# Optimization experiments

Hardware: AMD Instinct MI355X
Metric: run time of the kernel (lower is better)

Reference implementation:

```python
import jax, jax.numpy as jnp
import numpy as np

H = 64        # HIDDEN_DIM
V = 64        # VOCAB_SIZE
INNER = 16    # INNER_DIM
LR = 0.01     # INFERENCE_LR
B = 256
L = 2048
EPS = 1e-5    # LayerNorm eps (torch default)


def setup_inputs() -> dict:
    key = jax.random.key(0)
    ks = jax.random.split(key, 8)

    def lin(k, fi, fo):
        return jax.random.normal(k, (fi, fo), jnp.float32) / np.sqrt(fi).astype(np.float32)

    return {
        "seq": jax.random.randint(ks[0], (B, L), 0, V),
        "embed": jax.random.normal(ks[1], (V, H), jnp.float32) * 0.02,
        "ff_w1": lin(ks[2], H, 2 * H), "ff_b1": jnp.zeros((2 * H,), jnp.float32),
        "ff_w2": lin(ks[3], 2 * H, H), "ff_b2": jnp.zeros((H,), jnp.float32),
        "ln_g": jnp.ones((H,), jnp.float32), "ln_b": jnp.zeros((H,), jnp.float32),
        "w1": lin(ks[4], H, INNER), "b1": jnp.zeros((INNER,), jnp.float32),
        "w2": lin(ks[5], INNER, H), "b2": jnp.zeros((H,), jnp.float32),
        "out_w": lin(ks[6], H, V), "out_b": jnp.zeros((V,), jnp.float32),
    }


def _mlp(p, x):
    W1, B1, W2, B2 = p
    return jnp.maximum(x @ W1 + B1, 0.0) @ W2 + B2


def reference(seq, embed, ff_w1, ff_b1, ff_w2, ff_b2, ln_g, ln_b,
              w1, b1, w2, b2, out_w, out_b):
    # Encoder: embed -> residual FFN -> LayerNorm
    e = embed[seq]                                        # [B,L,H]
    ff = jnp.maximum(e @ ff_w1 + ff_b1, 0.0) @ ff_w2 + ff_b2
    h = e + ff
    mu = h.mean(-1, keepdims=True)
    var = ((h - mu) ** 2).mean(-1, keepdims=True)
    hs = (h - mu) / jnp.sqrt(var + EPS) * ln_g + ln_b     # [B,L,H]
    hs = jax.lax.stop_gradient(hs)                        # all TTT inputs are .detach()ed in torch

    T = (L - 2) // 2                                      # len(range(0, L-3, 2))
    idx = jnp.arange(T) * 2
    k_seq = hs[:, idx]                                    # [B,T,H]
    v_seq = hs[:, idx + 1]                                # [B,T,H]

    # base params copied via load_state_dict -> no grad connection
    p0 = tuple(jax.lax.stop_gradient(p) for p in (w1, b1, w2, b2))

    def ttt(kseq, vseq, qlast):
        def step(p, kv):
            k, v = kv
            g = jax.grad(lambda pp: jnp.mean((_mlp(pp, k) - v) ** 2))(p)
            return jax.tree_util.tree_map(lambda a, ga: a - LR * ga, p, g), None
        pf, _ = jax.lax.scan(step, p0, (kseq, vseq))
        return _mlp(pf, qlast)                            # [H]

    ctx = jax.vmap(ttt)(k_seq, v_seq, hs[:, -1])          # [B,H]
    ctx = jax.lax.stop_gradient(ctx)                      # torch builds ctx under no_grad
    return ctx @ out_w + out_b                            # [B,V]
```

## Files before the change

### kernel.cpp

```cpp
#include <hip/hip_runtime.h>

#define TSTEPS 1023
#define GAMMA  (0.01f / 32.0f)
#define EPSV   1e-5f

#define WS_HS 0
#define WS_G  4096
#define WS_Z0 8192

typedef float v2f __attribute__((ext_vector_type(2)));
typedef unsigned int v2u __attribute__((ext_vector_type(2)));

template<int CTRL>
__device__ __forceinline__ float dppmov(float x) {
    return __int_as_float(__builtin_amdgcn_update_dpp(0, __float_as_int(x), CTRL, 0xF, 0xF, true));
}
__device__ __forceinline__ v2u swap16(float a, float b) {
    return __builtin_amdgcn_permlane16_swap(__float_as_uint(a), __float_as_uint(b), false, false);
}
__device__ __forceinline__ v2u swap32(float a, float b) {
    return __builtin_amdgcn_permlane32_swap(__float_as_uint(a), __float_as_uint(b), false, false);
}
#define U2F(x) __uint_as_float(x)
#define PV(arr, j) (((j) & 1) ? arr[(j) >> 1].y : arr[(j) >> 1].x)

__global__ void hs_kernel(const float* __restrict__ embed,
                          const float* __restrict__ ffw1, const float* __restrict__ ffb1,
                          const float* __restrict__ ffw2, const float* __restrict__ ffb2,
                          const float* __restrict__ lng,  const float* __restrict__ lnb,
                          float* __restrict__ ws) {
    __shared__ float e[64];
    __shared__ float a1[128];
    int w = blockIdx.x;
    int tid = threadIdx.x;
    if (tid < 64) e[tid] = embed[w * 64 + tid];
    __syncthreads();
    float z1 = ffb1[tid];
    for (int x = 0; x < 64; ++x) z1 += e[x] * ffw1[x * 128 + tid];
    a1[tid] = fmaxf(z1, 0.0f);
    __syncthreads();
    if (tid < 64) {
        float f = ffb2[tid];
        for (int i = 0; i < 128; ++i) f += a1[i] * ffw2[i * 64 + tid];
        float hv = e[tid] + f;
        float s = hv;
#pragma unroll
        for (int m = 32; m >= 1; m >>= 1) s += __shfl_xor(s, m);
        float mu = s * (1.0f / 64.0f);
        float dv = hv - mu;
        float vs = dv * dv;
#pragma unroll
        for (int m = 32; m >= 1; m >>= 1) vs += __shfl_xor(vs, m);
        float rstd = 1.0f / sqrtf(vs * (1.0f / 64.0f) + EPSV);
        ws[WS_HS + w * 64 + tid] = dv * rstd * lng[tid] + lnb[tid];
    }
}

__global__ void gz_kernel(const float* __restrict__ w1, const float* __restrict__ b1,
                          float* __restrict__ ws) {
    __shared__ float row[64];
    int w = blockIdx.x, tid = threadIdx.x;
    row[tid] = ws[WS_HS + w * 64 + tid];
    __syncthreads();
    float g = 0.0f;
    for (int x = 0; x < 64; ++x) g += row[x] * ws[WS_HS + tid * 64 + x];
    ws[WS_G + w * 64 + tid] = GAMMA * g + GAMMA;
    if (tid < 16) {
        float z = b1[tid];
        for (int x = 0; x < 64; ++x) z += row[x] * w1[x * 16 + tid];
        ws[WS_Z0 + w * 16 + tid] = z;
    }
}

struct TTT2Smem {
    float hs[4096];
    float Gs[4096];
    int   sq[2048];
    __align__(16) float Z[2][512];
    float ybuf[2][2][64];
    float ctxp[2][64];
};

__device__ __forceinline__ void reduce8(const v2f* a2, const v2f* p2, v2f* dz2) {
    float q0 = PV(p2, 0) + dppmov<0xB1>(PV(p2, 4));
    float q1 = PV(p2, 1) + dppmov<0xB1>(PV(p2, 5));
    float q2 = PV(p2, 2) + dppmov<0xB1>(PV(p2, 6));
    float q3 = PV(p2, 3) + dppmov<0xB1>(PV(p2, 7));
    float rm0 = (a2[0].x > 0.0f) ? q0 : 0.0f;
    float rm1 = (a2[0].y > 0.0f) ? q1 : 0.0f;
    float rm2 = (a2[1].x > 0.0f) ? q2 : 0.0f;
    float rm3 = (a2[1].y > 0.0f) ? q3 : 0.0f;
    v2u f01 = swap16(rm0, rm1);
    const float F  = U2F(f01[0]) + U2F(f01[1]);
    v2u f23 = swap16(rm2, rm3);
    const float F2 = U2F(f23[0]) + U2F(f23[1]);
    v2u g01 = swap32(F, F2);
    float T = U2F(g01[0]) + U2F(g01[1]);
    T = T + dppmov<0x122>(T);
    T = T + dppmov<0x124>(T);
    T = T + dppmov<0x128>(T);
    v2u u01 = swap16(T, T);
    v2u v02 = swap32(U2F(u01[0]), U2F(u01[0]));
    v2u v13 = swap32(U2F(u01[1]), U2F(u01[1]));
    const float D0 = U2F(v02[0]);
    const float D2 = U2F(v02[1]);
    const float D1 = U2F(v13[0]);
    const float D3 = U2F(v13[1]);
    dz2[0] = {D0, D1};
    dz2[1] = {D2, D3};
    dz2[2] = {dppmov<0xB1>(D0), dppmov<0xB1>(D1)};
    dz2[3] = {dppmov<0xB1>(D2), dppmov<0xB1>(D3)};
}

__launch_bounds__(128, 1)
__global__ void ttt_kernel(const int* __restrict__ seq,
                           const float* __restrict__ w2, const float* __restrict__ b2i,
                           const float* __restrict__ outw, const float* __restrict__ outb,
                           const float* __restrict__ ws, float* __restrict__ out) {
    __shared__ TTT2Smem sm;

    const int b    = blockIdx.x;
    const int tid  = threadIdx.x;
    const int wv   = tid >> 6;
    const int lane = tid & 63;
    const int b0   = lane & 1;
    const int X    = b0 << 2;
    const int sl   = (lane >> 2) & 1;
    const bool wv0 = (wv == 0);

    {
        float4*       hv = (float4*)sm.hs;
        const float4* sv = (const float4*)(ws + WS_HS);
#pragma unroll
        for (int m = 0; m < 8; ++m) hv[m * 128 + tid] = sv[m * 128 + tid];
        float4*       gv = (float4*)sm.Gs;
        const float4* gs = (const float4*)(ws + WS_G);
#pragma unroll
        for (int m = 0; m < 8; ++m) gv[m * 128 + tid] = gs[m * 128 + tid];
        int4*       qv = (int4*)sm.sq;
        const int4* qs = (const int4*)(seq + b * 2048);
#pragma unroll
        for (int m = 0; m < 4; ++m) qv[m * 128 + tid] = qs[m * 128 + tid];
        const float* z0p = ws + WS_Z0 + lane * 16 + 8 * wv;
        float* zw = sm.Z[wv] + lane * 8;
        *(float4*)(zw + 4 * sl)       = *(const float4*)(z0p);
        *(float4*)(zw + 4 * (1 ^ sl)) = *(const float4*)(z0p + 4);
    }

    v2f W2p[4];
#pragma unroll
    for (int i = 0; i < 4; ++i) {
        v2f w;
        w.x = w2[(8 * wv + ((2 * i) ^ X)) * 64 + lane];
        w.y = w2[(8 * wv + ((2 * i + 1) ^ X)) * 64 + lane];
        W2p[i] = w;
    }
    float ybias = wv0 ? b2i[lane] : 0.0f;
    const float gma = wv0 ? GAMMA : 0.0f;
    __syncthreads();

    float* const Zw = sm.Z[wv];
    int tk = sm.sq[0];
    v2f z2[4];
    {
        const float* zb = Zw + tk * 8;
        const int x0 = (b0 ^ ((tk >> 2) & 1)) << 2;
        const float4 c0 = *(const float4*)(zb + x0);
        const float4 c1 = *(const float4*)(zb + (x0 ^ 4));
        z2[0] = {c0.x, c0.y}; z2[1] = {c0.z, c0.w};
        z2[2] = {c1.x, c1.y}; z2[3] = {c1.z, c1.w};
    }
    float4 ZrQ[2];
    v2f* Zv = (v2f*)ZrQ;
    {
        const float* zb = Zw + lane * 8;
        const int x0 = (b0 ^ sl) << 2;
        ZrQ[0] = *(const float4*)(zb + x0);
        ZrQ[1] = *(const float4*)(zb + (x0 ^ 4));
    }
    float vv = sm.hs[sm.sq[1] * 64 + lane];

    float4* const wp0 = (float4*)(Zw + lane * 8 + ((b0 ^ sl) << 2));
    float4* const wp1 = (float4*)(Zw + lane * 8 + (((b0 ^ sl) << 2) ^ 4));

    int2 pairT  = *(const int2*)(sm.sq + 2);
    int2 pairT1 = *(const int2*)(sm.sq + 4);

#pragma unroll 2
    for (int t = 0; t < TSTEPS - 1; ++t) {
        const int tkn = pairT.x;
        const int tvn = pairT.y;
        const int par = t & 1;

        const v2f zero2 = {0.0f, 0.0f};
        v2f a2[4];
#pragma unroll
        for (int i = 0; i < 4; ++i) a2[i] = __builtin_elementwise_max(z2[i], zero2);
        v2f acc0 = a2[0] * W2p[0] + a2[1] * W2p[1];
        v2f acc1 = a2[2] * W2p[2] + a2[3] * W2p[3];
        v2f accv = acc0 + acc1;
        const float ypart = ybias + accv.x + accv.y;

        sm.ybuf[par][wv][lane] = ypart;
        __syncthreads();
        const float yoth = sm.ybuf[par][wv ^ 1][lane];

        const float* zb = Zw + tkn * 8;
        const int x0 = (b0 ^ ((tkn >> 2) & 1)) << 2;
        const float4 e0 = *(const float4*)(zb + x0);
        const float4 e1 = *(const float4*)(zb + (x0 ^ 4));
        const float vnext = sm.hs[tvn * 64 + lane];
        const float cr = sm.Gs[tk * 64 + lane];
        const float cz = sm.Gs[tk * 64 + tkn];
        const int2 pairT2 = *(const int2*)(sm.sq + 2 * t + 6);

        const float d = (ypart + yoth) - vv;

        const v2f d2 = {d, d};
        v2f p2[4];
#pragma unroll
        for (int i = 0; i < 4; ++i) p2[i] = W2p[i] * d2;
        const float sd = GAMMA * d;
        ybias -= gma * d;
        const v2f sd2 = {sd, sd};
#pragma unroll
        for (int i = 0; i < 4; ++i) W2p[i] = W2p[i] - sd2 * a2[i];

        v2f dz2[4];
        reduce8(a2, p2, dz2);

        const v2f cr2 = {cr, cr}, cz2 = {cz, cz};
        const v2f zq2[4] = { {e0.x, e0.y}, {e0.z, e0.w}, {e1.x, e1.y}, {e1.z, e1.w} };
#pragma unroll
        for (int i = 0; i < 4; ++i) {
            Zv[i] = Zv[i] - cr2 * dz2[i];
            z2[i] = zq2[i] - cz2 * dz2[i];
        }
        *wp0 = ZrQ[0];
        *wp1 = ZrQ[1];

        vv = vnext;
        tk = tkn;
        pairT = pairT1;
        pairT1 = pairT2;
    }

    {
        const int tkn = pairT.y;
        const v2f zero2 = {0.0f, 0.0f};
        v2f a2[4];
#pragma unroll
        for (int i = 0; i < 4; ++i) a2[i] = __builtin_elementwise_max(z2[i], zero2);
        v2f acc0 = a2[0] * W2p[0] + a2[1] * W2p[1];
        v2f acc1 = a2[2] * W2p[2] + a2[3] * W2p[3];
        v2f accv = acc0 + acc1;
        const float ypart = ybias + accv.x + accv.y;

        sm.ybuf[0][wv][lane] = ypart;
        __syncthreads();
        const float yoth = sm.ybuf[0][wv ^ 1][lane];

        const float* zb = Zw + tkn * 8;
        const int x0 = (b0 ^ ((tkn >> 2) & 1)) << 2;
        const float4 e0 = *(const float4*)(zb + x0);
        const float4 e1 = *(const float4*)(zb + (x0 ^ 4));
        const float cz = sm.Gs[tk * 64 + tkn];

        const float d = (ypart + yoth) - vv;

        const v2f d2 = {d, d};
        v2f p2[4];
#pragma unroll
        for (int i = 0; i < 4; ++i) p2[i] = W2p[i] * d2;
        const float sd = GAMMA * d;
        ybias -= gma * d;
        const v2f sd2 = {sd, sd};
#pragma unroll
        for (int i = 0; i < 4; ++i) W2p[i] = W2p[i] - sd2 * a2[i];

        v2f dz2[4];
        reduce8(a2, p2, dz2);

        const v2f cz2 = {cz, cz};
        const v2f zq2[4] = { {e0.x, e0.y}, {e0.z, e0.w}, {e1.x, e1.y}, {e1.z, e1.w} };
#pragma unroll
        for (int i = 0; i < 4; ++i) z2[i] = zq2[i] - cz2 * dz2[i];
    }

    {
        const v2f zero2 = {0.0f, 0.0f};
        v2f acc = {0.0f, 0.0f};
#pragma unroll
        for (int i = 0; i < 4; ++i)
            acc = acc + __builtin_elementwise_max(z2[i], zero2) * W2p[i];
        sm.ctxp[wv][lane] = ybias + acc.x + acc.y;
    }
    __syncthreads();
    if (wv0) {
        float o = outb[lane];
        for (int hh = 0; hh < 64; ++hh)
            o += (sm.ctxp[0][hh] + sm.ctxp[1][hh]) * outw[hh * 64 + lane];
        out[b * 64 + lane] = o;
    }
}

extern "C" void kernel_launch(void* const* d_in, const int* in_sizes, int n_in,
                              void* d_out, int out_size, void* d_ws, size_t ws_size,
                              hipStream_t stream) {
    const int*   seq   = (const int*)d_in[0];
    const float* embed = (const float*)d_in[1];
    const float* ffw1  = (const float*)d_in[2];
    const float* ffb1  = (const float*)d_in[3];
    const float* ffw2  = (const float*)d_in[4];
    const float* ffb2  = (const float*)d_in[5];
    const float* lng   = (const float*)d_in[6];
    const float* lnb   = (const float*)d_in[7];
    const float* w1    = (const float*)d_in[8];
    const float* b1    = (const float*)d_in[9];
    const float* w2    = (const float*)d_in[10];
    const float* b2    = (const float*)d_in[11];
    const float* outw  = (const float*)d_in[12];
    const float* outb  = (const float*)d_in[13];
    float* ws  = (float*)d_ws;
    float* out = (float*)d_out;

    hipLaunchKernelGGL(hs_kernel, dim3(64), dim3(128), 0, stream,
                       embed, ffw1, ffb1, ffw2, ffb2, lng, lnb, ws);
    hipLaunchKernelGGL(gz_kernel, dim3(64), dim3(64), 0, stream, w1, b1, ws);
    hipLaunchKernelGGL(ttt_kernel, dim3(256), dim3(128), 0, stream,
                       seq, w2, b2, outw, outb, ws, out);
}
```

Baseline: 395.0 us.

## Split TTT inner dimension across four wavefronts instead of two

The per-sequence TTT kernel now uses 256 threads (4 wavefronts), so each wave owns 4 of the 16 inner units instead of 8. This halves per-wave arithmetic and shortens the cross-lane reduction on the serial per-step chain. The cost is a 4-way partial-sum exchange through shared memory at each step's barrier. The Z-table row update is also deferred to the next iteration so its LDS write overlaps the barrier wait.

```diff
diff --git a/kernel.cpp b/kernel.cpp
--- a/kernel.cpp
+++ b/kernel.cpp
@@ -22,7 +22,6 @@
     return __builtin_amdgcn_permlane32_swap(__float_as_uint(a), __float_as_uint(b), false, false);
 }
 #define U2F(x) __uint_as_float(x)
-#define PV(arr, j) (((j) & 1) ? arr[(j) >> 1].y : arr[(j) >> 1].x)
 
 __global__ void hs_kernel(const float* __restrict__ embed,
                           const float* __restrict__ ffw1, const float* __restrict__ ffb1,
@@ -72,87 +71,71 @@
     }
 }
 
-struct TTT2Smem {
+struct TTT4Smem {
     float hs[4096];
     float Gs[4096];
     int   sq[2048];
-    __align__(16) float Z[2][512];
-    float ybuf[2][2][64];
-    float ctxp[2][64];
+    __align__(16) float Z[4][256];
+    float ybuf[2][4][64];
+    float ctxp[4][64];
 };
 
-__device__ __forceinline__ void reduce8(const v2f* a2, const v2f* p2, v2f* dz2) {
-    float q0 = PV(p2, 0) + dppmov<0xB1>(PV(p2, 4));
-    float q1 = PV(p2, 1) + dppmov<0xB1>(PV(p2, 5));
-    float q2 = PV(p2, 2) + dppmov<0xB1>(PV(p2, 6));
-    float q3 = PV(p2, 3) + dppmov<0xB1>(PV(p2, 7));
+__device__ __forceinline__ void reduce4(const v2f* a2, const v2f* p2, v2f* dz2) {
+    float q0 = p2[0].x + dppmov<0xB1>(p2[1].x);
+    float q1 = p2[0].y + dppmov<0xB1>(p2[1].y);
     float rm0 = (a2[0].x > 0.0f) ? q0 : 0.0f;
     float rm1 = (a2[0].y > 0.0f) ? q1 : 0.0f;
-    float rm2 = (a2[1].x > 0.0f) ? q2 : 0.0f;
-    float rm3 = (a2[1].y > 0.0f) ? q3 : 0.0f;
     v2u f01 = swap16(rm0, rm1);
-    const float F  = U2F(f01[0]) + U2F(f01[1]);
-    v2u f23 = swap16(rm2, rm3);
-    const float F2 = U2F(f23[0]) + U2F(f23[1]);
-    v2u g01 = swap32(F, F2);
-    float T = U2F(g01[0]) + U2F(g01[1]);
+    float T = U2F(f01[0]) + U2F(f01[1]);
+    v2u g01 = swap32(T, T);
+    T = U2F(g01[0]) + U2F(g01[1]);
     T = T + dppmov<0x122>(T);
     T = T + dppmov<0x124>(T);
     T = T + dppmov<0x128>(T);
     v2u u01 = swap16(T, T);
-    v2u v02 = swap32(U2F(u01[0]), U2F(u01[0]));
-    v2u v13 = swap32(U2F(u01[1]), U2F(u01[1]));
-    const float D0 = U2F(v02[0]);
-    const float D2 = U2F(v02[1]);
-    const float D1 = U2F(v13[0]);
-    const float D3 = U2F(v13[1]);
-    dz2[0] = {D0, D1};
-    dz2[1] = {D2, D3};
-    dz2[2] = {dppmov<0xB1>(D0), dppmov<0xB1>(D1)};
-    dz2[3] = {dppmov<0xB1>(D2), dppmov<0xB1>(D3)};
-}
-
-__launch_bounds__(128, 1)
+    const float A0 = U2F(u01[0]);
+    const float A1 = U2F(u01[1]);
+    dz2[0] = {A0, A1};
+    dz2[1] = {dppmov<0xB1>(A0), dppmov<0xB1>(A1)};
+}
+
+__launch_bounds__(256, 1)
 __global__ void ttt_kernel(const int* __restrict__ seq,
                            const float* __restrict__ w2, const float* __restrict__ b2i,
                            const float* __restrict__ outw, const float* __restrict__ outb,
                            const float* __restrict__ ws, float* __restrict__ out) {
-    __shared__ TTT2Smem sm;
+    __shared__ TTT4Smem sm;
 
     const int b    = blockIdx.x;
     const int tid  = threadIdx.x;
     const int wv   = tid >> 6;
     const int lane = tid & 63;
     const int b0   = lane & 1;
-    const int X    = b0 << 2;
-    const int sl   = (lane >> 2) & 1;
+    const int X    = b0 << 1;
     const bool wv0 = (wv == 0);
 
     {
         float4*       hv = (float4*)sm.hs;
         const float4* sv = (const float4*)(ws + WS_HS);
 #pragma unroll
-        for (int m = 0; m < 8; ++m) hv[m * 128 + tid] = sv[m * 128 + tid];
+        for (int m = 0; m < 4; ++m) hv[m * 256 + tid] = sv[m * 256 + tid];
         float4*       gv = (float4*)sm.Gs;
         const float4* gs = (const float4*)(ws + WS_G);
 #pragma unroll
-        for (int m = 0; m < 8; ++m) gv[m * 128 + tid] = gs[m * 128 + tid];
+        for (int m = 0; m < 4; ++m) gv[m * 256 + tid] = gs[m * 256 + tid];
         int4*       qv = (int4*)sm.sq;
         const int4* qs = (const int4*)(seq + b * 2048);
 #pragma unroll
-        for (int m = 0; m < 4; ++m) qv[m * 128 + tid] = qs[m * 128 + tid];
-        const float* z0p = ws + WS_Z0 + lane * 16 + 8 * wv;
-        float* zw = sm.Z[wv] + lane * 8;
-        *(float4*)(zw + 4 * sl)       = *(const float4*)(z0p);
-        *(float4*)(zw + 4 * (1 ^ sl)) = *(const float4*)(z0p + 4);
-    }
-
-    v2f W2p[4];
-#pragma unroll
-    for (int i = 0; i < 4; ++i) {
+        for (int m = 0; m < 2; ++m) qv[m * 256 + tid] = qs[m * 256 + tid];
+        *(float4*)(sm.Z[wv] + lane * 4) = *(const float4*)(ws + WS_Z0 + lane * 16 + 4 * wv);
+    }
+
+    v2f W2p[2];
+#pragma unroll
+    for (int i = 0; i < 2; ++i) {
         v2f w;
-        w.x = w2[(8 * wv + ((2 * i) ^ X)) * 64 + lane];
-        w.y = w2[(8 * wv + ((2 * i + 1) ^ X)) * 64 + lane];
+        w.x = w2[(4 * wv + ((2 * i) ^ X)) * 64 + lane];
+        w.y = w2[(4 * wv + ((2 * i + 1) ^ X)) * 64 + lane];
         W2p[i] = w;
     }
     float ybias = wv0 ? b2i[lane] : 0.0f;
@@ -161,27 +144,25 @@
 
     float* const Zw = sm.Z[wv];
     int tk = sm.sq[0];
-    v2f z2[4];
-    {
-        const float* zb = Zw + tk * 8;
-        const int x0 = (b0 ^ ((tk >> 2) & 1)) << 2;
-        const float4 c0 = *(const float4*)(zb + x0);
-        const float4 c1 = *(const float4*)(zb + (x0 ^ 4));
-        z2[0] = {c0.x, c0.y}; z2[1] = {c0.z, c0.w};
-        z2[2] = {c1.x, c1.y}; z2[3] = {c1.z, c1.w};
-    }
-    float4 ZrQ[2];
-    v2f* Zv = (v2f*)ZrQ;
-    {
-        const float* zb = Zw + lane * 8;
-        const int x0 = (b0 ^ sl) << 2;
-        ZrQ[0] = *(const float4*)(zb + x0);
-        ZrQ[1] = *(const float4*)(zb + (x0 ^ 4));
+    v2f z2[2];
+    {
+        const float* zb = Zw + tk * 4;
+        z2[0] = *(const v2f*)(zb + (b0 << 1));
+        z2[1] = *(const v2f*)(zb + ((b0 << 1) ^ 2));
+    }
+    v2f Zv[2];
+    {
+        const float* zb = Zw + lane * 4;
+        Zv[0] = *(const v2f*)(zb + (b0 << 1));
+        Zv[1] = *(const v2f*)(zb + ((b0 << 1) ^ 2));
     }
     float vv = sm.hs[sm.sq[1] * 64 + lane];
 
-    float4* const wp0 = (float4*)(Zw + lane * 8 + ((b0 ^ sl) << 2));
-    float4* const wp1 = (float4*)(Zw + lane * 8 + (((b0 ^ sl) << 2) ^ 4));
+    v2f* const wp0 = (v2f*)(Zw + lane * 4 + (b0 << 1));
+    v2f* const wp1 = (v2f*)(Zw + lane * 4 + ((b0 << 1) ^ 2));
+
+    v2f dzp[2] = {{0.0f, 0.0f}, {0.0f, 0.0f}};
+    float crp = 0.0f;
 
     int2 pairT  = *(const int2*)(sm.sq + 2);
     int2 pairT1 = *(const int2*)(sm.sq + 4);
@@ -193,51 +174,54 @@
         const int par = t & 1;
 
         const v2f zero2 = {0.0f, 0.0f};
-        v2f a2[4];
-#pragma unroll
-        for (int i = 0; i < 4; ++i) a2[i] = __builtin_elementwise_max(z2[i], zero2);
-        v2f acc0 = a2[0] * W2p[0] + a2[1] * W2p[1];
-        v2f acc1 = a2[2] * W2p[2] + a2[3] * W2p[3];
-        v2f accv = acc0 + acc1;
+        v2f a2[2];
+        a2[0] = __builtin_elementwise_max(z2[0], zero2);
+        a2[1] = __builtin_elementwise_max(z2[1], zero2);
+        v2f accv = a2[0] * W2p[0] + a2[1] * W2p[1];
         const float ypart = ybias + accv.x + accv.y;
 
         sm.ybuf[par][wv][lane] = ypart;
         __syncthreads();
-        const float yoth = sm.ybuf[par][wv ^ 1][lane];
-
-        const float* zb = Zw + tkn * 8;
-        const int x0 = (b0 ^ ((tkn >> 2) & 1)) << 2;
-        const float4 e0 = *(const float4*)(zb + x0);
-        const float4 e1 = *(const float4*)(zb + (x0 ^ 4));
+        const float y0 = sm.ybuf[par][0][lane];
+        const float y1 = sm.ybuf[par][1][lane];
+        const float y2 = sm.ybuf[par][2][lane];
+        const float y3 = sm.ybuf[par][3][lane];
+
+        const v2f crp2 = {crp, crp};
+        Zv[0] = Zv[0] - crp2 * dzp[0];
+        Zv[1] = Zv[1] - crp2 * dzp[1];
+        *wp0 = Zv[0];
+        *wp1 = Zv[1];
+        const float* zb = Zw + tkn * 4;
+        const v2f e0 = *(const v2f*)(zb + (b0 << 1));
+        const v2f e1 = *(const v2f*)(zb + ((b0 << 1) ^ 2));
         const float vnext = sm.hs[tvn * 64 + lane];
-        const float cr = sm.Gs[tk * 64 + lane];
-        const float cz = sm.Gs[tk * 64 + tkn];
+        const float crc = sm.Gs[tk * 64 + lane];
+        const float cz  = sm.Gs[tk * 64 + tkn];
         const int2 pairT2 = *(const int2*)(sm.sq + 2 * t + 6);
 
-        const float d = (ypart + yoth) - vv;
+        const float d = ((y0 + y1) + (y2 + y3)) - vv;
 
         const v2f d2 = {d, d};
-        v2f p2[4];
-#pragma unroll
-        for (int i = 0; i < 4; ++i) p2[i] = W2p[i] * d2;
+        v2f p2[2];
+        p2[0] = W2p[0] * d2;
+        p2[1] = W2p[1] * d2;
         const float sd = GAMMA * d;
         ybias -= gma * d;
         const v2f sd2 = {sd, sd};
-#pragma unroll
-        for (int i = 0; i < 4; ++i) W2p[i] = W2p[i] - sd2 * a2[i];
-
-        v2f dz2[4];
-        reduce8(a2, p2, dz2);
-
-        const v2f cr2 = {cr, cr}, cz2 = {cz, cz};
-        const v2f zq2[4] = { {e0.x, e0.y}, {e0.z, e0.w}, {e1.x, e1.y}, {e1.z, e1.w} };
-#pragma unroll
-        for (int i = 0; i < 4; ++i) {
-            Zv[i] = Zv[i] - cr2 * dz2[i];
-            z2[i] = zq2[i] - cz2 * dz2[i];
-        }
-        *wp0 = ZrQ[0];
-        *wp1 = ZrQ[1];
+        W2p[0] = W2p[0] - sd2 * a2[0];
+        W2p[1] = W2p[1] - sd2 * a2[1];
+
+        v2f dz2[2];
+        reduce4(a2, p2, dz2);
+
+        const v2f cz2 = {cz, cz};
+        z2[0] = e0 - cz2 * dz2[0];
+        z2[1] = e1 - cz2 * dz2[1];
+
+        dzp[0] = dz2[0];
+        dzp[1] = dz2[1];
+        crp = crc;
 
         vv = vnext;
         tk = tkn;
@@ -248,58 +232,62 @@
     {
         const int tkn = pairT.y;
         const v2f zero2 = {0.0f, 0.0f};
-        v2f a2[4];
-#pragma unroll
-        for (int i = 0; i < 4; ++i) a2[i] = __builtin_elementwise_max(z2[i], zero2);
-        v2f acc0 = a2[0] * W2p[0] + a2[1] * W2p[1];
-        v2f acc1 = a2[2] * W2p[2] + a2[3] * W2p[3];
-        v2f accv = acc0 + acc1;
+        v2f a2[2];
+        a2[0] = __builtin_elementwise_max(z2[0], zero2);
+        a2[1] = __builtin_elementwise_max(z2[1], zero2);
+        v2f accv = a2[0] * W2p[0] + a2[1] * W2p[1];
         const float ypart = ybias + accv.x + accv.y;
 
         sm.ybuf[0][wv][lane] = ypart;
         __syncthreads();
-        const float yoth = sm.ybuf[0][wv ^ 1][lane];
-
-        const float* zb = Zw + tkn * 8;
-        const int x0 = (b0 ^ ((tkn >> 2) & 1)) << 2;
-        const float4 e0 = *(const float4*)(zb + x0);
-        const float4 e1 = *(const float4*)(zb + (x0 ^ 4));
+        const float y0 = sm.ybuf[0][0][lane];
+        const float y1 = sm.ybuf[0][1][lane];
+        const float y2 = sm.ybuf[0][2][lane];
+        const float y3 = sm.ybuf[0][3][lane];
+
+        const v2f crp2 = {crp, crp};
+        Zv[0] = Zv[0] - crp2 * dzp[0];
+        Zv[1] = Zv[1] - crp2 * dzp[1];
+        *wp0 = Zv[0];
+        *wp1 = Zv[1];
+
+        const float* zb = Zw + tkn * 4;
+        const v2f e0 = *(const v2f*)(zb + (b0 << 1));
+        const v2f e1 = *(const v2f*)(zb + ((b0 << 1) ^ 2));
         const float cz = sm.Gs[tk * 64 + tkn];
 
-        const float d = (ypart + yoth) - vv;
+        const float d = ((y0 + y1) + (y2 + y3)) - vv;
 
         const v2f d2 = {d, d};
-        v2f p2[4];
-#pragma unroll
-        for (int i = 0; i < 4; ++i) p2[i] = W2p[i] * d2;
+        v2f p2[2];
+        p2[0] = W2p[0] * d2;
+        p2[1] = W2p[1] * d2;
         const float sd = GAMMA * d;
         ybias -= gma * d;
         const v2f sd2 = {sd, sd};
-#pragma unroll
-        for (int i = 0; i < 4; ++i) W2p[i] = W2p[i] - sd2 * a2[i];
-
-        v2f dz2[4];
-        reduce8(a2, p2, dz2);
+        W2p[0] = W2p[0] - sd2 * a2[0];
+        W2p[1] = W2p[1] - sd2 * a2[1];
+
+        v2f dz2[2];
+        reduce4(a2, p2, dz2);
 
         const v2f cz2 = {cz, cz};
-        const v2f zq2[4] = { {e0.x, e0.y}, {e0.z, e0.w}, {e1.x, e1.y}, {e1.z, e1.w} };
-#pragma unroll
-        for (int i = 0; i < 4; ++i) z2[i] = zq2[i] - cz2 * dz2[i];
+        z2[0] = e0 - cz2 * dz2[0];
+        z2[1] = e1 - cz2 * dz2[1];
     }
 
     {
         const v2f zero2 = {0.0f, 0.0f};
-        v2f acc = {0.0f, 0.0f};
-#pragma unroll
-        for (int i = 0; i < 4; ++i)
-            acc = acc + __builtin_elementwise_max(z2[i], zero2) * W2p[i];
+        v2f acc = __builtin_elementwise_max(z2[0], zero2) * W2p[0]
+                + __builtin_elementwise_max(z2[1], zero2) * W2p[1];
         sm.ctxp[wv][lane] = ybias + acc.x + acc.y;
     }
     __syncthreads();
     if (wv0) {
         float o = outb[lane];
         for (int hh = 0; hh < 64; ++hh)
-            o += (sm.ctxp[0][hh] + sm.ctxp[1][hh]) * outw[hh * 64 + lane];
+            o += (sm.ctxp[0][hh] + sm.ctxp[1][hh] + sm.ctxp[2][hh] + sm.ctxp[3][hh])
+                 * outw[hh * 64 + lane];
         out[b * 64 + lane] = o;
     }
 }
@@ -327,6 +315,6 @@
     hipLaunchKernelGGL(hs_kernel, dim3(64), dim3(128), 0, stream,
                        embed, ffw1, ffb1, ffw2, ffb2, lng, lnb, ws);
     hipLaunchKernelGGL(gz_kernel, dim3(64), dim3(64), 0, stream, w1, b1, ws);
-    hipLaunchKernelGGL(ttt_kernel, dim3(256), dim3(128), 0, stream,
+    hipLaunchKernelGGL(ttt_kernel, dim3(256), dim3(256), 0, stream,
                        seq, w2, b2, outw, outb, ws, out);
 }
```

Result: faster. 366.6 us (-7.2%).
